# Optimization experiments

Measured on AMD Instinct MI355X. Metric: run time of the kernel, lower is better.

The kernel has to match this reference:

```python
import jax, jax.numpy as jnp
import numpy as np


def setup_inputs() -> dict:
    key = jax.random.key(0)
    k1, k2 = jax.random.split(key)
    x_in = jax.random.normal(k1, (8, 16384, 64), dtype=jnp.float32)
    codebook = jax.random.normal(k2, (512, 64), dtype=jnp.float32)
    return {"x_in": x_in, "codebook": codebook}


def reference(x_in, codebook):
    # Euclidean distances x_in [B,N,D] vs codebook [K,D] -> [B,N,K]
    x_sq = jnp.sum(x_in * x_in, axis=-1, keepdims=True)            # [B,N,1]
    e_sq = jnp.sum(codebook * codebook, axis=-1)                   # [K]
    cross = jnp.einsum('bnd,kd->bnk', x_in, codebook)              # [B,N,K]
    d2 = x_sq + e_sq[None, None, :] - 2.0 * cross
    distances = jnp.sqrt(jnp.maximum(d2, 0.0))
    # argmin with keepdim, as in extract_indices
    indices = jnp.argmin(distances, axis=2, keepdims=True)         # [B,N,1]
    # apply_codebook: embedding lookup -> [B,N,1,D]
    quantized = codebook[indices]
    return quantized
```

## Files before the change

kernel.cpp:

```cpp
#include <hip/hip_runtime.h>

#define D    64
#define K    512
#define QTOT (8 * 16384)
#define THR  0.008f

typedef __attribute__((ext_vector_type(8))) short short8;
typedef __attribute__((ext_vector_type(4))) short short4v;
typedef __attribute__((ext_vector_type(4))) float f32x4;

__device__ __forceinline__ unsigned short f2bf(float f) {
    unsigned u = __builtin_bit_cast(unsigned, f);
    u = u + 0x7FFFu + ((u >> 16) & 1u);
    return (unsigned short)(u >> 16);
}
__device__ __forceinline__ float bf2f(unsigned short h) {
    unsigned u = ((unsigned)h) << 16;
    return __builtin_bit_cast(float, u);
}

__global__ __launch_bounds__(512) void prep2_kernel(const float* __restrict__ cb,
        float* __restrict__ esq, unsigned short* __restrict__ eh2,
        unsigned short* __restrict__ el2) {
    const int tid = threadIdx.x;
    const float4* cbv4 = (const float4*)cb;
    for (int c = tid; c < (K * D) / 4; c += 512) {
        float4 v = cbv4[c];
        float vv[4] = {v.x, v.y, v.z, v.w};
        short4v hi, lo;
        #pragma unroll
        for (int j = 0; j < 4; ++j) {
            unsigned short hb = f2bf(vv[j]);
            float hf = bf2f(hb);
            unsigned short lb = f2bf(vv[j] - hf);
            hi[j] = (short)f2bf(-2.0f * hf);
            lo[j] = (short)f2bf(-2.0f * bf2f(lb));
        }
        ((short4v*)eh2)[c] = hi;
        ((short4v*)el2)[c] = lo;
    }
    const float4* rp = (const float4*)(cb + (size_t)tid * D);
    float s = 0.f;
    #pragma unroll
    for (int i = 0; i < 16; ++i) {
        float4 v = rp[i];
        s = fmaf(v.x, v.x, s); s = fmaf(v.y, v.y, s);
        s = fmaf(v.z, v.z, s); s = fmaf(v.w, v.w, s);
    }
    esq[tid] = s;
}

__global__ __launch_bounds__(1024) void vq_mfma7(
        const float* __restrict__ x, const float* __restrict__ cb,
        const float* __restrict__ g_esq, const unsigned short* __restrict__ eh2,
        const unsigned short* __restrict__ el2, float* __restrict__ out) {

    __shared__ unsigned short s_e[2][K * D];
    __shared__ float s_esq[K];

    const int tid  = threadIdx.x;
    const int lane = tid & 63;
    const int qrow = lane & 15;
    const int kg   = lane >> 4;
    const int kg4  = kg * 4;
    const int wv   = __builtin_amdgcn_readfirstlane(tid >> 6);
    const int qw   = blockIdx.x * 512 + wv * 32;

    for (int c = tid; c < (K * D) / 8; c += 1024) {
        short8 hv = ((const short8*)eh2)[c];
        short8 lv = ((const short8*)el2)[c];
        int byteoff = c * 16;
        int row     = byteoff >> 7;
        int addr    = byteoff ^ ((row & 7) << 4);
        *(short8*)((char*)s_e[0] + addr) = hv;
        *(short8*)((char*)s_e[1] + addr) = lv;
    }
    if (tid < K) s_esq[tid] = g_esq[tid];
    __syncthreads();

    short8 xh[2][2], xl[2][2];
    #pragma unroll
    for (int qt = 0; qt < 2; ++qt) {
        #pragma unroll
        for (int h = 0; h < 2; ++h) {
            const float* p = x + (size_t)(qw + qt * 16 + qrow) * D + h * 32 + kg * 8;
            float4 v0 = *(const float4*)p;
            float4 v1 = *(const float4*)(p + 4);
            float vv[8] = {v0.x, v0.y, v0.z, v0.w, v1.x, v1.y, v1.z, v1.w};
            short8 th, tl;
            #pragma unroll
            for (int j = 0; j < 8; ++j) {
                unsigned short hb = f2bf(vv[j]);
                th[j] = (short)hb;
                tl[j] = (short)f2bf(vv[j] - bf2f(hb));
            }
            xh[qt][h] = th;
            xl[qt][h] = tl;
        }
    }

    float m1[2], m2[2];
    int   i1[2];
    #pragma unroll
    for (int qt = 0; qt < 2; ++qt) { m1[qt] = 3.4e38f; m2[qt] = 3.4e38f; i1[qt] = 0; }

    const int swz = (qrow & 7) << 4;
    const int ob  = qrow * 128 + kg * 16;
    const char* ph = (const char*)s_e[0];
    const char* pl = (const char*)s_e[1];
    const int o0 = ob ^ swz;
    const int o1 = (ob + 64) ^ swz;
    const float* pq = s_esq + kg4;

    #pragma unroll
    for (int t = 0; t < 32; ++t) {
        short8 eh0 = *(const short8*)(ph + o0 + t * 2048);
        short8 eh1 = *(const short8*)(ph + o1 + t * 2048);
        short8 el0 = *(const short8*)(pl + o0 + t * 2048);
        short8 el1 = *(const short8*)(pl + o1 + t * 2048);
        f32x4 eqv  = *(const f32x4*)(pq + t * 16);

        #pragma unroll
        for (int qt = 0; qt < 2; ++qt) {
            f32x4 acc = eqv;
            acc = __builtin_amdgcn_mfma_f32_16x16x32_bf16(eh0, xh[qt][0], acc, 0, 0, 0);
            acc = __builtin_amdgcn_mfma_f32_16x16x32_bf16(eh1, xh[qt][1], acc, 0, 0, 0);
            acc = __builtin_amdgcn_mfma_f32_16x16x32_bf16(eh0, xl[qt][0], acc, 0, 0, 0);
            acc = __builtin_amdgcn_mfma_f32_16x16x32_bf16(eh1, xl[qt][1], acc, 0, 0, 0);
            acc = __builtin_amdgcn_mfma_f32_16x16x32_bf16(el0, xh[qt][0], acc, 0, 0, 0);
            acc = __builtin_amdgcn_mfma_f32_16x16x32_bf16(el1, xh[qt][1], acc, 0, 0, 0);
            #pragma unroll
            for (int r = 0; r < 4; ++r) {
                float dd = acc[r];
                int   kc = (t * 16) | (kg4 + r);
                bool  lt = dd < m1[qt];
                m2[qt] = lt ? m1[qt] : fminf(m2[qt], dd);
                m1[qt] = lt ? dd : m1[qt];
                i1[qt] = lt ? kc : i1[qt];
            }
        }
    }

    #pragma unroll
    for (int qt = 0; qt < 2; ++qt) {
        #pragma unroll
        for (int off = 16; off <= 32; off <<= 1) {
            float om1 = __shfl_xor(m1[qt], off, 64);
            float om2 = __shfl_xor(m2[qt], off, 64);
            int   oi  = __shfl_xor(i1[qt], off, 64);
            bool  lt  = om1 < m1[qt];
            float loser = lt ? m1[qt] : om1;
            m2[qt] = fminf(fminf(m2[qt], om2), loser);
            m1[qt] = lt ? om1 : m1[qt];
            i1[qt] = lt ? oi  : i1[qt];
        }
    }

    #pragma unroll
    for (int qt = 0; qt < 2; ++qt) {
        bool flag = (m2[qt] - m1[qt]) <= THR;
        unsigned long long mask = __ballot(flag && (lane < 16));
        while (mask) {
            int ql = __ffsll(mask) - 1;
            mask &= mask - 1;
            int qf = qw + qt * 16 + ql;
            const float* xq = x + (size_t)qf * D;
            float bb = 3.4e38f;
            int   bq = 0;
            #pragma unroll 1
            for (int c0 = 0; c0 < 8; ++c0) {
                int kc = lane * 8 + c0;
                const float4* ep = (const float4*)(cb + (size_t)kc * D);
                float a = 0.f;
                #pragma unroll
                for (int i = 0; i < 16; ++i) {
                    float4 e = ep[i];
                    a = fmaf(xq[4 * i + 0], e.x, a);
                    a = fmaf(xq[4 * i + 1], e.y, a);
                    a = fmaf(xq[4 * i + 2], e.z, a);
                    a = fmaf(xq[4 * i + 3], e.w, a);
                }
                float dd = fmaf(-2.f, a, s_esq[kc]);
                if (dd < bb) { bb = dd; bq = kc; }
            }
            #pragma unroll
            for (int off = 1; off < 64; off <<= 1) {
                float ob = __shfl_xor(bb, off, 64);
                int   oq = __shfl_xor(bq, off, 64);
                if (ob < bb || (ob == bb && oq < bq)) { bb = ob; bq = oq; }
            }
            if (qrow == ql) i1[qt] = bq;
        }
    }

    #pragma unroll
    for (int qt = 0; qt < 2; ++qt) {
        size_t q = (size_t)(qw + qt * 16 + qrow);
        const float4* src = (const float4*)(cb + (size_t)i1[qt] * D) + kg * 4;
        float4*       dst = (float4*)(out + q * D) + kg * 4;
        #pragma unroll
        for (int s = 0; s < 4; ++s) dst[s] = src[s];
    }
}

__global__ __launch_bounds__(512) void vq_mfma(
        const float* __restrict__ x, const float* __restrict__ cb,
        float* __restrict__ out) {

    __shared__ unsigned short s_e[2][K * D];
    __shared__ float s_esq[K];

    const int tid  = threadIdx.x;
    const int lane = tid & 63;
    const int qrow = lane & 15;
    const int kg   = lane >> 4;
    const int wv   = __builtin_amdgcn_readfirstlane(tid >> 6);
    const int qw   = blockIdx.x * 512 + wv * 64;

    const float4* cbv4 = (const float4*)cb;
    for (int c = tid; c < (K * D) / 4; c += 512) {
        float4 v = cbv4[c];
        float vv[4] = {v.x, v.y, v.z, v.w};
        short4v hi, lo;
        #pragma unroll
        for (int j = 0; j < 4; ++j) {
            unsigned short hb = f2bf(vv[j]);
            hi[j] = (short)hb;
            lo[j] = (short)f2bf(vv[j] - bf2f(hb));
        }
        int byteoff = c * 8;
        int row     = byteoff >> 7;
        int addr    = byteoff ^ ((row & 7) << 4);
        *(short4v*)((char*)s_e[0] + addr) = hi;
        *(short4v*)((char*)s_e[1] + addr) = lo;
    }
    {
        float s = 0.f;
        #pragma unroll
        for (int d = 0; d < D; ++d) {
            float v = cb[tid * D + d];
            s = fmaf(v, v, s);
        }
        s_esq[tid] = s;
    }
    __syncthreads();

    short8 xh[4][2], xl[4][2];
    #pragma unroll
    for (int qt = 0; qt < 4; ++qt) {
        #pragma unroll
        for (int h = 0; h < 2; ++h) {
            const float* p = x + (size_t)(qw + qt * 16 + qrow) * D + h * 32 + kg * 8;
            float4 v0 = *(const float4*)p;
            float4 v1 = *(const float4*)(p + 4);
            float vv[8] = {v0.x, v0.y, v0.z, v0.w, v1.x, v1.y, v1.z, v1.w};
            short8 th, tl;
            #pragma unroll
            for (int j = 0; j < 8; ++j) {
                unsigned short hb = f2bf(vv[j]);
                th[j] = (short)hb;
                tl[j] = (short)f2bf(vv[j] - bf2f(hb));
            }
            xh[qt][h] = th;
            xl[qt][h] = tl;
        }
    }

    float m1[4], m2[4];
    int   i1[4];
    #pragma unroll
    for (int qt = 0; qt < 4; ++qt) { m1[qt] = 3.4e38f; m2[qt] = 3.4e38f; i1[qt] = 0; }

    const f32x4 zacc = {0.f, 0.f, 0.f, 0.f};

    for (int t = 0; t < 32; ++t) {
        const int row  = t * 16 + qrow;
        const int swz  = (row & 7) << 4;
        const int off0 = row * 128 + kg * 16;
        short8 eh0 = *(const short8*)((const char*)s_e[0] + ((off0     ) ^ swz));
        short8 eh1 = *(const short8*)((const char*)s_e[0] + ((off0 + 64) ^ swz));
        short8 el0 = *(const short8*)((const char*)s_e[1] + ((off0     ) ^ swz));
        short8 el1 = *(const short8*)((const char*)s_e[1] + ((off0 + 64) ^ swz));
        f32x4 eq = *(const f32x4*)(s_esq + t * 16 + kg * 4);

        #pragma unroll
        for (int qt = 0; qt < 4; ++qt) {
            f32x4 acc;
            asm volatile(
                "s_nop 3\n\t"
                "v_mfma_f32_16x16x32_bf16 %0, %1, %5, %9\n\t"
                "v_mfma_f32_16x16x32_bf16 %0, %2, %6, %0\n\t"
                "v_mfma_f32_16x16x32_bf16 %0, %1, %7, %0\n\t"
                "v_mfma_f32_16x16x32_bf16 %0, %2, %8, %0\n\t"
                "v_mfma_f32_16x16x32_bf16 %0, %3, %5, %0\n\t"
                "v_mfma_f32_16x16x32_bf16 %0, %4, %6, %0\n\t"
                "s_nop 7\n\t"
                "s_nop 7"
                : "=&v"(acc)
                : "v"(eh0), "v"(eh1), "v"(el0), "v"(el1),
                  "v"(xh[qt][0]), "v"(xh[qt][1]), "v"(xl[qt][0]), "v"(xl[qt][1]),
                  "v"(zacc));
            #pragma unroll
            for (int r = 0; r < 4; ++r) {
                float dd = fmaf(-2.f, acc[r], eq[r]);
                int   kc = t * 16 + kg * 4 + r;
                bool  lt = dd < m1[qt];
                m2[qt] = lt ? m1[qt] : fminf(m2[qt], dd);
                m1[qt] = lt ? dd : m1[qt];
                i1[qt] = lt ? kc : i1[qt];
            }
        }
    }

    #pragma unroll
    for (int qt = 0; qt < 4; ++qt) {
        #pragma unroll
        for (int off = 16; off <= 32; off <<= 1) {
            float om1 = __shfl_xor(m1[qt], off, 64);
            float om2 = __shfl_xor(m2[qt], off, 64);
            int   oi  = __shfl_xor(i1[qt], off, 64);
            bool  lt  = om1 < m1[qt];
            float loser = lt ? m1[qt] : om1;
            m2[qt] = fminf(fminf(m2[qt], om2), loser);
            m1[qt] = lt ? om1 : m1[qt];
            i1[qt] = lt ? oi  : i1[qt];
        }
    }

    #pragma unroll
    for (int qt = 0; qt < 4; ++qt) {
        bool flag = (m2[qt] - m1[qt]) <= 0.008f;
        unsigned long long mask = __ballot(flag && (lane < 16));
        while (mask) {
            int ql = __ffsll(mask) - 1;
            mask &= mask - 1;
            int qf = qw + qt * 16 + ql;
            const float* xq = x + (size_t)qf * D;
            float bb = 3.4e38f;
            int   bq = 0;
            #pragma unroll 1
            for (int c0 = 0; c0 < 8; ++c0) {
                int kc = lane * 8 + c0;
                const float4* ep = (const float4*)(cb + (size_t)kc * D);
                float a = 0.f;
                #pragma unroll
                for (int i = 0; i < 16; ++i) {
                    float4 e = ep[i];
                    a = fmaf(xq[4 * i + 0], e.x, a);
                    a = fmaf(xq[4 * i + 1], e.y, a);
                    a = fmaf(xq[4 * i + 2], e.z, a);
                    a = fmaf(xq[4 * i + 3], e.w, a);
                }
                float dd = fmaf(-2.f, a, s_esq[kc]);
                if (dd < bb) { bb = dd; bq = kc; }
            }
            #pragma unroll
            for (int off = 1; off < 64; off <<= 1) {
                float ob = __shfl_xor(bb, off, 64);
                int   oq = __shfl_xor(bq, off, 64);
                if (ob < bb || (ob == bb && oq < bq)) { bb = ob; bq = oq; }
            }
            if (qrow == ql) i1[qt] = bq;
        }
    }

    #pragma unroll
    for (int qt = 0; qt < 4; ++qt) {
        size_t q = (size_t)(qw + qt * 16 + qrow);
        const float4* src = (const float4*)(cb + (size_t)i1[qt] * D) + kg * 4;
        float4*       dst = (float4*)(out + q * D) + kg * 4;
        #pragma unroll
        for (int s = 0; s < 4; ++s) dst[s] = src[s];
    }
}

extern "C" void kernel_launch(void* const* d_in, const int* in_sizes, int n_in,
                              void* d_out, int out_size, void* d_ws, size_t ws_size,
                              hipStream_t stream) {
    const float* x   = (const float*)d_in[0];
    const float* cb  = (const float*)d_in[1];
    float*       out = (float*)d_out;

    const size_t need = 2048 + (size_t)K * D * 2 * 2;
    if (ws_size >= need) {
        float*          esq = (float*)d_ws;
        unsigned short* eh2 = (unsigned short*)((char*)d_ws + 2048);
        unsigned short* el2 = (unsigned short*)((char*)d_ws + 2048 + K * D * 2);
        prep2_kernel<<<1, 512, 0, stream>>>(cb, esq, eh2, el2);
        vq_mfma7<<<QTOT / 512, 1024, 0, stream>>>(x, cb, esq, eh2, el2, out);
    } else {
        vq_mfma<<<QTOT / 512, 512, 0, stream>>>(x, cb, out);
    }
}
```

Before: 57.44 us.

## Switch distance MFMA to fp16 split-x with single codebook, smaller query tiles

Replaces the bf16 hi/lo split (six MFMAs per tile) with fp16, where the codebook is stored only as a single fp16 term and x is split into hi/lo fp16 parts, giving four MFMAs per tile. LDS holds only one codebook copy, which halves shared memory per block. Each wave now handles 16 queries instead of 32 and the grid doubles. The near-tie threshold is raised so more queries fall back to the exact fp32 rescan, which trades extra fallback work for the precision lost in the codebook.

```diff
diff --git a/kernel.cpp b/kernel.cpp
--- a/kernel.cpp
+++ b/kernel.cpp
@@ -3,11 +3,13 @@
 #define D    64
 #define K    512
 #define QTOT (8 * 16384)
-#define THR  0.008f
-
-typedef __attribute__((ext_vector_type(8))) short short8;
-typedef __attribute__((ext_vector_type(4))) short short4v;
-typedef __attribute__((ext_vector_type(4))) float f32x4;
+#define THR  0.05f
+
+typedef __attribute__((ext_vector_type(8))) short    short8;
+typedef __attribute__((ext_vector_type(4))) short    short4v;
+typedef __attribute__((ext_vector_type(8))) _Float16 half8;
+typedef __attribute__((ext_vector_type(4))) _Float16 half4;
+typedef __attribute__((ext_vector_type(4))) float    f32x4;
 
 __device__ __forceinline__ unsigned short f2bf(float f) {
     unsigned u = __builtin_bit_cast(unsigned, f);
@@ -19,25 +21,18 @@
     return __builtin_bit_cast(float, u);
 }
 
-__global__ __launch_bounds__(512) void prep2_kernel(const float* __restrict__ cb,
-        float* __restrict__ esq, unsigned short* __restrict__ eh2,
-        unsigned short* __restrict__ el2) {
+__global__ __launch_bounds__(512) void prep3_kernel(const float* __restrict__ cb,
+        float* __restrict__ esq, _Float16* __restrict__ eh2) {
     const int tid = threadIdx.x;
     const float4* cbv4 = (const float4*)cb;
     for (int c = tid; c < (K * D) / 4; c += 512) {
         float4 v = cbv4[c];
-        float vv[4] = {v.x, v.y, v.z, v.w};
-        short4v hi, lo;
-        #pragma unroll
-        for (int j = 0; j < 4; ++j) {
-            unsigned short hb = f2bf(vv[j]);
-            float hf = bf2f(hb);
-            unsigned short lb = f2bf(vv[j] - hf);
-            hi[j] = (short)f2bf(-2.0f * hf);
-            lo[j] = (short)f2bf(-2.0f * bf2f(lb));
-        }
-        ((short4v*)eh2)[c] = hi;
-        ((short4v*)el2)[c] = lo;
+        half4 h;
+        h[0] = (_Float16)(-2.0f * v.x);
+        h[1] = (_Float16)(-2.0f * v.y);
+        h[2] = (_Float16)(-2.0f * v.z);
+        h[3] = (_Float16)(-2.0f * v.w);
+        ((half4*)eh2)[c] = h;
     }
     const float4* rp = (const float4*)(cb + (size_t)tid * D);
     float s = 0.f;
@@ -50,12 +45,12 @@
     esq[tid] = s;
 }
 
-__global__ __launch_bounds__(1024) void vq_mfma7(
+__global__ __launch_bounds__(1024, 8) void vq_f16(
         const float* __restrict__ x, const float* __restrict__ cb,
-        const float* __restrict__ g_esq, const unsigned short* __restrict__ eh2,
-        const unsigned short* __restrict__ el2, float* __restrict__ out) {
-
-    __shared__ unsigned short s_e[2][K * D];
+        const float* __restrict__ g_esq, const _Float16* __restrict__ eh2,
+        float* __restrict__ out) {
+
+    __shared__ unsigned short s_eh[K * D];
     __shared__ float s_esq[K];
 
     const int tid  = threadIdx.x;
@@ -64,106 +59,91 @@
     const int kg   = lane >> 4;
     const int kg4  = kg * 4;
     const int wv   = __builtin_amdgcn_readfirstlane(tid >> 6);
-    const int qw   = blockIdx.x * 512 + wv * 32;
+    const int qw   = blockIdx.x * 256 + wv * 16;
+    const size_t q = (size_t)(qw + qrow);
 
     for (int c = tid; c < (K * D) / 8; c += 1024) {
         short8 hv = ((const short8*)eh2)[c];
-        short8 lv = ((const short8*)el2)[c];
         int byteoff = c * 16;
         int row     = byteoff >> 7;
         int addr    = byteoff ^ ((row & 7) << 4);
-        *(short8*)((char*)s_e[0] + addr) = hv;
-        *(short8*)((char*)s_e[1] + addr) = lv;
+        *(short8*)((char*)s_eh + addr) = hv;
     }
     if (tid < K) s_esq[tid] = g_esq[tid];
     __syncthreads();
 
-    short8 xh[2][2], xl[2][2];
-    #pragma unroll
-    for (int qt = 0; qt < 2; ++qt) {
+    half8 xh0, xh1, xl0, xl1;
+    {
+        const float* p = x + q * D + kg * 8;
         #pragma unroll
         for (int h = 0; h < 2; ++h) {
-            const float* p = x + (size_t)(qw + qt * 16 + qrow) * D + h * 32 + kg * 8;
-            float4 v0 = *(const float4*)p;
-            float4 v1 = *(const float4*)(p + 4);
+            float4 v0 = *(const float4*)(p + h * 32);
+            float4 v1 = *(const float4*)(p + h * 32 + 4);
             float vv[8] = {v0.x, v0.y, v0.z, v0.w, v1.x, v1.y, v1.z, v1.w};
-            short8 th, tl;
+            half8 th, tl;
             #pragma unroll
             for (int j = 0; j < 8; ++j) {
-                unsigned short hb = f2bf(vv[j]);
-                th[j] = (short)hb;
-                tl[j] = (short)f2bf(vv[j] - bf2f(hb));
-            }
-            xh[qt][h] = th;
-            xl[qt][h] = tl;
-        }
-    }
-
-    float m1[2], m2[2];
-    int   i1[2];
-    #pragma unroll
-    for (int qt = 0; qt < 2; ++qt) { m1[qt] = 3.4e38f; m2[qt] = 3.4e38f; i1[qt] = 0; }
+                _Float16 hb = (_Float16)vv[j];
+                th[j] = hb;
+                tl[j] = (_Float16)(vv[j] - (float)hb);
+            }
+            if (h == 0) { xh0 = th; xl0 = tl; }
+            else        { xh1 = th; xl1 = tl; }
+        }
+    }
+
+    float m1 = 3.4e38f, m2 = 3.4e38f;
+    int   i1 = 0;
 
     const int swz = (qrow & 7) << 4;
     const int ob  = qrow * 128 + kg * 16;
-    const char* ph = (const char*)s_e[0];
-    const char* pl = (const char*)s_e[1];
-    const int o0 = ob ^ swz;
-    const int o1 = (ob + 64) ^ swz;
+    const int o0  = ob ^ swz;
+    const int o1  = (ob + 64) ^ swz;
+    const char*  ph = (const char*)s_eh;
     const float* pq = s_esq + kg4;
 
     #pragma unroll
     for (int t = 0; t < 32; ++t) {
-        short8 eh0 = *(const short8*)(ph + o0 + t * 2048);
-        short8 eh1 = *(const short8*)(ph + o1 + t * 2048);
-        short8 el0 = *(const short8*)(pl + o0 + t * 2048);
-        short8 el1 = *(const short8*)(pl + o1 + t * 2048);
-        f32x4 eqv  = *(const f32x4*)(pq + t * 16);
-
-        #pragma unroll
-        for (int qt = 0; qt < 2; ++qt) {
-            f32x4 acc = eqv;
-            acc = __builtin_amdgcn_mfma_f32_16x16x32_bf16(eh0, xh[qt][0], acc, 0, 0, 0);
-            acc = __builtin_amdgcn_mfma_f32_16x16x32_bf16(eh1, xh[qt][1], acc, 0, 0, 0);
-            acc = __builtin_amdgcn_mfma_f32_16x16x32_bf16(eh0, xl[qt][0], acc, 0, 0, 0);
-            acc = __builtin_amdgcn_mfma_f32_16x16x32_bf16(eh1, xl[qt][1], acc, 0, 0, 0);
-            acc = __builtin_amdgcn_mfma_f32_16x16x32_bf16(el0, xh[qt][0], acc, 0, 0, 0);
-            acc = __builtin_amdgcn_mfma_f32_16x16x32_bf16(el1, xh[qt][1], acc, 0, 0, 0);
-            #pragma unroll
-            for (int r = 0; r < 4; ++r) {
-                float dd = acc[r];
-                int   kc = (t * 16) | (kg4 + r);
-                bool  lt = dd < m1[qt];
-                m2[qt] = lt ? m1[qt] : fminf(m2[qt], dd);
-                m1[qt] = lt ? dd : m1[qt];
-                i1[qt] = lt ? kc : i1[qt];
-            }
-        }
-    }
-
-    #pragma unroll
-    for (int qt = 0; qt < 2; ++qt) {
-        #pragma unroll
-        for (int off = 16; off <= 32; off <<= 1) {
-            float om1 = __shfl_xor(m1[qt], off, 64);
-            float om2 = __shfl_xor(m2[qt], off, 64);
-            int   oi  = __shfl_xor(i1[qt], off, 64);
-            bool  lt  = om1 < m1[qt];
-            float loser = lt ? m1[qt] : om1;
-            m2[qt] = fminf(fminf(m2[qt], om2), loser);
-            m1[qt] = lt ? om1 : m1[qt];
-            i1[qt] = lt ? oi  : i1[qt];
-        }
-    }
-
-    #pragma unroll
-    for (int qt = 0; qt < 2; ++qt) {
-        bool flag = (m2[qt] - m1[qt]) <= THR;
+        half8 eh0 = *(const half8*)(ph + o0 + t * 2048);
+        half8 eh1 = *(const half8*)(ph + o1 + t * 2048);
+        f32x4 eqv = *(const f32x4*)(pq + t * 16);
+
+        f32x4 acc = eqv;
+        acc = __builtin_amdgcn_mfma_f32_16x16x32_f16(eh0, xh0, acc, 0, 0, 0);
+        acc = __builtin_amdgcn_mfma_f32_16x16x32_f16(eh1, xh1, acc, 0, 0, 0);
+        acc = __builtin_amdgcn_mfma_f32_16x16x32_f16(eh0, xl0, acc, 0, 0, 0);
+        acc = __builtin_amdgcn_mfma_f32_16x16x32_f16(eh1, xl1, acc, 0, 0, 0);
+
+        #pragma unroll
+        for (int r = 0; r < 4; ++r) {
+            float dd = acc[r];
+            int   kc = (t * 16) | (kg4 + r);
+            bool  lt = dd < m1;
+            m2 = lt ? m1 : fminf(m2, dd);
+            m1 = lt ? dd : m1;
+            i1 = lt ? kc : i1;
+        }
+    }
+
+    #pragma unroll
+    for (int off = 16; off <= 32; off <<= 1) {
+        float om1 = __shfl_xor(m1, off, 64);
+        float om2 = __shfl_xor(m2, off, 64);
+        int   oi  = __shfl_xor(i1, off, 64);
+        bool  lt  = om1 < m1;
+        float loser = lt ? m1 : om1;
+        m2 = fminf(fminf(m2, om2), loser);
+        m1 = lt ? om1 : m1;
+        i1 = lt ? oi  : i1;
+    }
+
+    {
+        bool flag = (m2 - m1) <= THR;
         unsigned long long mask = __ballot(flag && (lane < 16));
         while (mask) {
             int ql = __ffsll(mask) - 1;
             mask &= mask - 1;
-            int qf = qw + qt * 16 + ql;
+            int qf = qw + ql;
             const float* xq = x + (size_t)qf * D;
             float bb = 3.4e38f;
             int   bq = 0;
@@ -189,14 +169,12 @@
                 int   oq = __shfl_xor(bq, off, 64);
                 if (ob < bb || (ob == bb && oq < bq)) { bb = ob; bq = oq; }
             }
-            if (qrow == ql) i1[qt] = bq;
-        }
-    }
-
-    #pragma unroll
-    for (int qt = 0; qt < 2; ++qt) {
-        size_t q = (size_t)(qw + qt * 16 + qrow);
-        const float4* src = (const float4*)(cb + (size_t)i1[qt] * D) + kg * 4;
+            if (qrow == ql) i1 = bq;
+        }
+    }
+
+    {
+        const float4* src = (const float4*)(cb + (size_t)i1 * D) + kg * 4;
         float4*       dst = (float4*)(out + q * D) + kg * 4;
         #pragma unroll
         for (int s = 0; s < 4; ++s) dst[s] = src[s];
@@ -381,13 +359,12 @@
     const float* cb  = (const float*)d_in[1];
     float*       out = (float*)d_out;
 
-    const size_t need = 2048 + (size_t)K * D * 2 * 2;
+    const size_t need = 2048 + (size_t)K * D * 2;
     if (ws_size >= need) {
-        float*          esq = (float*)d_ws;
-        unsigned short* eh2 = (unsigned short*)((char*)d_ws + 2048);
-        unsigned short* el2 = (unsigned short*)((char*)d_ws + 2048 + K * D * 2);
-        prep2_kernel<<<1, 512, 0, stream>>>(cb, esq, eh2, el2);
-        vq_mfma7<<<QTOT / 512, 1024, 0, stream>>>(x, cb, esq, eh2, el2, out);
+        float*     esq = (float*)d_ws;
+        _Float16*  eh2 = (_Float16*)((char*)d_ws + 2048);
+        prep3_kernel<<<1, 512, 0, stream>>>(cb, esq, eh2);
+        vq_f16<<<QTOT / 256, 1024, 0, stream>>>(x, cb, esq, eh2, out);
     } else {
         vq_mfma<<<QTOT / 512, 512, 0, stream>>>(x, cb, out);
     }
```

Result: slower. 81.30 us (+41.5%).

## Parallelize codebook prep across blocks and restructure exact-distance fallback

Applied to the files above, without the earlier changes.

The codebook preprocessing kernel now runs on 8 blocks instead of 1, so its serial latency before the main kernel is shorter. The top-2 tracking replaces selects with fminf/fmaxf. The exact fp32 fallback for ambiguous queries is rewritten: each 16-lane group splits a codebook row across lanes, computes the squared difference directly and reduces it with shuffles. This gives coalesced float4 codebook reads instead of per-lane scalar x loads and row-strided codebook reads. The fallback now compares true squared distances rather than esq - 2*dot, which may change tie behaviour slightly.

```diff
diff --git a/kernel.cpp b/kernel.cpp
--- a/kernel.cpp
+++ b/kernel.cpp
@@ -19,12 +19,13 @@
     return __builtin_bit_cast(float, u);
 }
 
-__global__ __launch_bounds__(512) void prep2_kernel(const float* __restrict__ cb,
+__global__ __launch_bounds__(512) void prep2b_kernel(const float* __restrict__ cb,
         float* __restrict__ esq, unsigned short* __restrict__ eh2,
         unsigned short* __restrict__ el2) {
     const int tid = threadIdx.x;
+    const int b   = blockIdx.x;
     const float4* cbv4 = (const float4*)cb;
-    for (int c = tid; c < (K * D) / 4; c += 512) {
+    for (int c = b * 512 + tid; c < (K * D) / 4; c += 4096) {
         float4 v = cbv4[c];
         float vv[4] = {v.x, v.y, v.z, v.w};
         short4v hi, lo;
@@ -39,18 +40,21 @@
         ((short4v*)eh2)[c] = hi;
         ((short4v*)el2)[c] = lo;
     }
-    const float4* rp = (const float4*)(cb + (size_t)tid * D);
-    float s = 0.f;
-    #pragma unroll
-    for (int i = 0; i < 16; ++i) {
-        float4 v = rp[i];
-        s = fmaf(v.x, v.x, s); s = fmaf(v.y, v.y, s);
-        s = fmaf(v.z, v.z, s); s = fmaf(v.w, v.w, s);
-    }
-    esq[tid] = s;
-}
-
-__global__ __launch_bounds__(1024) void vq_mfma7(
+    if (tid < 64) {
+        const int row = b * 64 + tid;
+        const float4* rp = (const float4*)(cb + (size_t)row * D);
+        float s = 0.f;
+        #pragma unroll
+        for (int i = 0; i < 16; ++i) {
+            float4 v = rp[i];
+            s = fmaf(v.x, v.x, s); s = fmaf(v.y, v.y, s);
+            s = fmaf(v.z, v.z, s); s = fmaf(v.w, v.w, s);
+        }
+        esq[row] = s;
+    }
+}
+
+__global__ __launch_bounds__(1024) void vq_mfma8(
         const float* __restrict__ x, const float* __restrict__ cb,
         const float* __restrict__ g_esq, const unsigned short* __restrict__ eh2,
         const unsigned short* __restrict__ el2, float* __restrict__ out) {
@@ -134,8 +138,8 @@
                 float dd = acc[r];
                 int   kc = (t * 16) | (kg4 + r);
                 bool  lt = dd < m1[qt];
-                m2[qt] = lt ? m1[qt] : fminf(m2[qt], dd);
-                m1[qt] = lt ? dd : m1[qt];
+                m2[qt] = fminf(fmaxf(m1[qt], dd), m2[qt]);
+                m1[qt] = fminf(m1[qt], dd);
                 i1[qt] = lt ? kc : i1[qt];
             }
         }
@@ -165,26 +169,29 @@
             mask &= mask - 1;
             int qf = qw + qt * 16 + ql;
             const float* xq = x + (size_t)qf * D;
+            float4 xv = *(const float4*)(xq + qrow * 4);
             float bb = 3.4e38f;
             int   bq = 0;
-            #pragma unroll 1
-            for (int c0 = 0; c0 < 8; ++c0) {
-                int kc = lane * 8 + c0;
-                const float4* ep = (const float4*)(cb + (size_t)kc * D);
-                float a = 0.f;
-                #pragma unroll
-                for (int i = 0; i < 16; ++i) {
-                    float4 e = ep[i];
-                    a = fmaf(xq[4 * i + 0], e.x, a);
-                    a = fmaf(xq[4 * i + 1], e.y, a);
-                    a = fmaf(xq[4 * i + 2], e.z, a);
-                    a = fmaf(xq[4 * i + 3], e.w, a);
-                }
-                float dd = fmaf(-2.f, a, s_esq[kc]);
-                if (dd < bb) { bb = dd; bq = kc; }
-            }
-            #pragma unroll
-            for (int off = 1; off < 64; off <<= 1) {
+            #pragma unroll 4
+            for (int c0 = 0; c0 < 128; ++c0) {
+                int c = c0 * 4 + kg;
+                float4 ev = *(const float4*)(cb + (size_t)c * D + qrow * 4);
+                float d0 = xv.x - ev.x;
+                float d1 = xv.y - ev.y;
+                float d2 = xv.z - ev.z;
+                float d3 = xv.w - ev.w;
+                float s  = d0 * d0;
+                s = fmaf(d1, d1, s);
+                s = fmaf(d2, d2, s);
+                s = fmaf(d3, d3, s);
+                s += __shfl_xor(s, 1, 64);
+                s += __shfl_xor(s, 2, 64);
+                s += __shfl_xor(s, 4, 64);
+                s += __shfl_xor(s, 8, 64);
+                if (s < bb) { bb = s; bq = c; }
+            }
+            #pragma unroll
+            for (int off = 16; off <= 32; off <<= 1) {
                 float ob = __shfl_xor(bb, off, 64);
                 int   oq = __shfl_xor(bq, off, 64);
                 if (ob < bb || (ob == bb && oq < bq)) { bb = ob; bq = oq; }
@@ -386,8 +393,8 @@
         float*          esq = (float*)d_ws;
         unsigned short* eh2 = (unsigned short*)((char*)d_ws + 2048);
         unsigned short* el2 = (unsigned short*)((char*)d_ws + 2048 + K * D * 2);
-        prep2_kernel<<<1, 512, 0, stream>>>(cb, esq, eh2, el2);
-        vq_mfma7<<<QTOT / 512, 1024, 0, stream>>>(x, cb, esq, eh2, el2, out);
+        prep2b_kernel<<<8, 512, 0, stream>>>(cb, esq, eh2, el2);
+        vq_mfma8<<<QTOT / 512, 1024, 0, stream>>>(x, cb, esq, eh2, el2, out);
     } else {
         vq_mfma<<<QTOT / 512, 512, 0, stream>>>(x, cb, out);
     }
```

Measured after the change: 63.51 us. 10.6% more time.
